# Optimization experiments

Hardware: AMD Instinct MI355X
Metric: run time of the kernel (lower is better)

Reference implementation:

```python
import jax, jax.numpy as jnp
import numpy as np

THETA = 0.5
LEAF_SIZE = 32
N_ATOMS = 8192
N_GRAPHS = 2


def _build_tree(pos_np, indices):
    # Mirrors OpenBoundaryTreeLongRangeKernel._build_tree (octree split at bbox center).
    local = pos_np[indices]
    cmin = local.min(axis=0)
    cmax = local.max(axis=0)
    center = 0.5 * (cmin + cmax)
    half = float((cmax - cmin).max() * 0.5)
    node = {"indices": indices, "iset": set(indices), "center": center,
            "half": half, "children": [], "cid": -1}
    if len(indices) <= LEAF_SIZE:
        return node
    bins = {}
    for i in indices:
        p = pos_np[i]
        key = (int(p[0] >= center[0]), int(p[1] >= center[1]), int(p[2] >= center[2]))
        bins.setdefault(key, []).append(i)
    if len(bins) <= 1:
        return node  # degenerate split -> treated as leaf (is_leaf == no children)
    node["children"] = [_build_tree(pos_np, ci) for ci in bins.values()]
    return node


def _plan(pos_np, batch_np, n_graphs, soft):
    # Host-side Barnes-Hut traversal (the torch original does this with .item() syncs).
    # Emits flat (target, source) direct pairs and (target, cluster) monopole pairs.
    direct_t, direct_s, clus_t, clus_c = [], [], [], []
    clusters = []
    for g in range(n_graphs):
        idx = np.nonzero(batch_np == g)[0]
        if idx.size == 0:
            continue
        root = _build_tree(pos_np, [int(i) for i in idx])
        for t in idx:
            t = int(t)
            tpos = pos_np[t]
            stack = [root]
            while stack:
                node = stack.pop()
                if not node["children"]:  # leaf: direct near-field sum
                    for s in node["indices"]:
                        if s != t:
                            direct_t.append(t)
                            direct_s.append(s)
                    continue
                d = tpos - node["center"]
                dist = float(np.sqrt((d * d).sum() + soft * soft))
                diam = max(2.0 * node["half"], 1e-9)
                if (t not in node["iset"]) and (diam / dist < THETA):
                    if node["cid"] < 0:
                        node["cid"] = len(clusters)
                        clusters.append(node["indices"])
                    clus_t.append(t)
                    clus_c.append(node["cid"])
                else:
                    stack.extend(node["children"])
    if clusters:
        midx = np.concatenate([np.asarray(c, dtype=np.int32) for c in clusters])
        mseg = np.concatenate([np.full(len(c), i, np.int32) for i, c in enumerate(clusters)])
        mcnt = np.asarray([len(c) for c in clusters], dtype=np.float32)
    else:
        midx = np.zeros((0,), np.int32)
        mseg = np.zeros((0,), np.int32)
        mcnt = np.ones((1,), np.float32)
    return (np.asarray(direct_t, np.int32), np.asarray(direct_s, np.int32),
            np.asarray(clus_t, np.int32), np.asarray(clus_c, np.int32),
            midx, mseg, mcnt, max(len(clusters), 1))


def _energy(pos, source, screening, softening, plan, n_atoms):
    # Vectorized, differentiable evaluation of the planned interactions.
    dt, ds, ct, cc, midx, mseg, mcnt, n_clusters = plan
    soft2 = softening * softening
    phi = jnp.zeros((n_atoms,), dtype=pos.dtype)
    if dt.size:
        delta = pos[dt] - pos[ds]                       # [P,3]
        r = jnp.sqrt(jnp.sum(delta * delta, axis=-1) + soft2)
        phi = phi + jax.ops.segment_sum(source[ds] * jnp.exp(-screening * r) / r,
                                        dt, num_segments=n_atoms)
    if ct.size:
        q = jax.ops.segment_sum(source[midx], mseg, num_segments=n_clusters)
        center = (jax.ops.segment_sum(pos[midx], mseg, num_segments=n_clusters)
                  / jnp.asarray(mcnt)[:, None])          # differentiable cluster mean
        delta = pos[ct] - center[cc]                    # [C,3]
        r = jnp.sqrt(jnp.sum(delta * delta, axis=-1) + soft2)
        phi = phi + jax.ops.segment_sum(q[cc] * jnp.exp(-screening * r) / r,
                                        ct, num_segments=n_atoms)
    return 0.5 * (source * phi)[:, None]                # [N,1], energy_partition='potential'


def setup_inputs() -> dict:
    key = jax.random.key(0)
    k1, k2, k3 = jax.random.split(key, 3)
    pos = jax.random.normal(k1, (N_ATOMS, 3), dtype=jnp.float32) * 6.0
    batch = jnp.sort(jax.random.randint(k2, (N_ATOMS,), 0, N_GRAPHS)).astype(jnp.int32)
    cell = jnp.zeros((N_GRAPHS, 3, 3), dtype=jnp.float32)
    source = jax.random.normal(k3, (N_ATOMS,), dtype=jnp.float32)
    screening = jnp.float32(0.5)
    softening = jnp.float32(0.1)
    return {"pos": pos, "batch": batch, "cell": cell, "source": source,
            "screening": screening, "softening": softening}


def reference(pos, batch, cell, source, screening, softening):
    pos_np = np.asarray(pos, dtype=np.float32)
    batch_np = np.asarray(batch)
    plan = _plan(pos_np, batch_np, int(cell.shape[0]), float(np.asarray(softening)))
    return _energy(pos, source, screening, softening, plan, pos.shape[0])
```

## Files before the change

kernel.cpp:

```cpp
#include <hip/hip_runtime.h>

#define LEAF_SZ 32
#define MAXN 16384
#define MAXNODES 65536
#define ARENA_BASE 32768
#define MAXG 64
#define NQ 1024
#define BGRID 128
#define LCAP 256
#define LSTK 192
#define BSTK 96
#define WQCAP 256
#define NW0 16

struct __align__(64) TNode { int4 meta; float4 c4; float4 m4; float4 pad; };

__device__ int    g_perm[MAXN];
__device__ int    g_ptmp[MAXN];
__device__ float4 g_p4[MAXN];
__device__ float4 g_t4[MAXN];
__device__ int    g_nstart[MAXNODES];
__device__ int    g_nend[MAXNODES];
__device__ TNode  g_nodes[MAXNODES];
__device__ int    g_root[MAXG];
__device__ int    g_ncount;
__device__ int    g_lrange[4];

struct NodeSh {
    float  mn[4][3], mx[4][3];
    double sx[4], sy[4], sz[4], sq[4];
    int    c8[4][8];
    int    cur[8];
    float  cc[3];
    int    info;
    int    base, num;
    int    tot[8], offk[8];
};

__device__ __forceinline__ void process_node2(NodeSh& sh, int n, int st, int en)
{
    const int tid  = threadIdx.x;
    const int wid  = tid >> 6;
    const int lane = tid & 63;
    const int cnt = en - st;

    float mnx = 3.402823466e38f, mny = mnx, mnz = mnx;
    float mxx = -mnx, mxy = -mnx, mxz = -mnx;
    double sx = 0.0, sy = 0.0, sz = 0.0, sq = 0.0;
    for (int j = st + tid; j < en; j += 256) {
        float4 p = g_p4[j];
        mnx = fminf(mnx, p.x); mny = fminf(mny, p.y); mnz = fminf(mnz, p.z);
        mxx = fmaxf(mxx, p.x); mxy = fmaxf(mxy, p.y); mxz = fmaxf(mxz, p.z);
        sx += (double)p.x; sy += (double)p.y; sz += (double)p.z; sq += (double)p.w;
    }
    for (int o = 1; o < 64; o <<= 1) {
        mnx = fminf(mnx, __shfl_xor(mnx, o));
        mny = fminf(mny, __shfl_xor(mny, o));
        mnz = fminf(mnz, __shfl_xor(mnz, o));
        mxx = fmaxf(mxx, __shfl_xor(mxx, o));
        mxy = fmaxf(mxy, __shfl_xor(mxy, o));
        mxz = fmaxf(mxz, __shfl_xor(mxz, o));
        sx += __shfl_xor(sx, o);
        sy += __shfl_xor(sy, o);
        sz += __shfl_xor(sz, o);
        sq += __shfl_xor(sq, o);
    }
    if (lane == 0) {
        sh.mn[wid][0] = mnx; sh.mn[wid][1] = mny; sh.mn[wid][2] = mnz;
        sh.mx[wid][0] = mxx; sh.mx[wid][1] = mxy; sh.mx[wid][2] = mxz;
        sh.sx[wid] = sx; sh.sy[wid] = sy; sh.sz[wid] = sz; sh.sq[wid] = sq;
    }
    __syncthreads();
    if (tid == 0) {
        float a0 = sh.mn[0][0], a1 = sh.mn[0][1], a2 = sh.mn[0][2];
        float b0 = sh.mx[0][0], b1 = sh.mx[0][1], b2 = sh.mx[0][2];
        double tx = sh.sx[0], ty = sh.sy[0], tz = sh.sz[0], tq = sh.sq[0];
        for (int w = 1; w < 4; ++w) {
            a0 = fminf(a0, sh.mn[w][0]); a1 = fminf(a1, sh.mn[w][1]); a2 = fminf(a2, sh.mn[w][2]);
            b0 = fmaxf(b0, sh.mx[w][0]); b1 = fmaxf(b1, sh.mx[w][1]); b2 = fmaxf(b2, sh.mx[w][2]);
            tx += sh.sx[w]; ty += sh.sy[w]; tz += sh.sz[w]; tq += sh.sq[w];
        }
        float cx = 0.5f * (a0 + b0), cy = 0.5f * (a1 + b1), cz = 0.5f * (a2 + b2);
        g_nodes[n].c4 = make_float4(cx, cy, cz, 0.5f * fmaxf(fmaxf(b0 - a0, b1 - a1), b2 - a2));
        const float fc = (float)cnt;
        g_nodes[n].m4 = make_float4((float)tx / fc, (float)ty / fc, (float)tz / fc, (float)tq);
        sh.cc[0] = cx; sh.cc[1] = cy; sh.cc[2] = cz;
        if (cnt <= LEAF_SZ) { g_nodes[n].meta = make_int4(st, en, 0, 0); sh.info = -1; }
        else sh.info = 0;
    }
    __syncthreads();
    if (sh.info < 0) return;
    const float cx = sh.cc[0], cy = sh.cc[1], cz = sh.cc[2];

    int c8[8] = {0,0,0,0,0,0,0,0};
    for (int j = st + tid; j < en; j += 256) {
        float4 p = g_p4[j];
        int oct = (p.x >= cx ? 1 : 0) | (p.y >= cy ? 2 : 0) | (p.z >= cz ? 4 : 0);
        c8[oct]++;
    }
    #pragma unroll
    for (int k = 0; k < 8; ++k)
        for (int o = 1; o < 64; o <<= 1)
            c8[k] += __shfl_xor(c8[k], o);
    if (lane == 0)
        #pragma unroll
        for (int k = 0; k < 8; ++k) sh.c8[wid][k] = c8[k];
    __syncthreads();
    if (tid == 0) {
        int tot[8], nonempty = 0;
        #pragma unroll
        for (int k = 0; k < 8; ++k) {
            tot[k] = sh.c8[0][k] + sh.c8[1][k] + sh.c8[2][k] + sh.c8[3][k];
            nonempty += (tot[k] > 0) ? 1 : 0;
        }
        if (nonempty <= 1) { g_nodes[n].meta = make_int4(st, en, 0, 0); sh.info = -1; }
        else {
            int base = atomicAdd(&g_ncount, nonempty);
            int acc = st, ci = base;
            #pragma unroll
            for (int k = 0; k < 8; ++k) {
                sh.cur[k] = acc;
                sh.offk[k] = acc - st;
                sh.tot[k] = tot[k];
                if (tot[k] > 0) { g_nstart[ci] = acc; g_nend[ci] = acc + tot[k]; ++ci; }
                acc += tot[k];
            }
            g_nodes[n].meta = make_int4(st, en, base, nonempty);
            sh.base = base; sh.num = nonempty; sh.info = 1;
        }
    }
    __syncthreads();
    if (sh.info < 0) return;

    for (int j = st + tid; j < en; j += 256) {
        float4 p = g_p4[j];
        int id = g_perm[j];
        int oct = (p.x >= cx ? 1 : 0) | (p.y >= cy ? 2 : 0) | (p.z >= cz ? 4 : 0);
        int pdst = atomicAdd(&sh.cur[oct], 1);
        g_ptmp[pdst] = id; g_t4[pdst] = p;
    }
    __syncthreads();
    for (int j = st + tid; j < en; j += 256) {
        g_perm[j] = g_ptmp[j];
        g_p4[j]   = g_t4[j];
    }
    __syncthreads();
}

__global__ __launch_bounds__(1024)
void level0_kernel(const float* __restrict__ pos, const float* __restrict__ src,
                   const int* __restrict__ batch, int N, int n_graphs)
{
    __shared__ int    s_first[MAXG], s_end[MAXG];
    __shared__ float  s_mn[NW0][3], s_mx[NW0][3];
    __shared__ double s_sx[NW0], s_sy[NW0], s_sz[NW0], s_sq[NW0];
    __shared__ int    s_c8[NW0][8];
    __shared__ int    s_cur[8];
    __shared__ float  s_cc[3];
    __shared__ int    s_info;
    const int tid = threadIdx.x, wid = tid >> 6, lane = tid & 63;
    const int ng = (n_graphs < MAXG) ? n_graphs : MAXG;

    for (int g = tid; g < MAXG; g += 1024) { s_first[g] = -1; s_end[g] = 0; }
    __syncthreads();
    for (int i = tid; i < N; i += 1024) {
        int b = batch[i];
        if (i == 0     || batch[i-1] != b) s_first[b] = i;
        if (i == N - 1 || batch[i+1] != b) s_end[b]   = i + 1;
    }
    __syncthreads();

    const int g = blockIdx.x;
    int nc = 0, myroot = -1;
    for (int q = 0; q < ng; ++q)
        if (s_first[q] >= 0) { if (q == g) myroot = nc; ++nc; }
    const int nb = nc + 8 * ng;

    if (g == 0 && tid == 0) {
        int r = 0;
        for (int q = 0; q < ng; ++q) {
            if (s_first[q] >= 0) g_root[q] = r++;
            else {
                g_root[q] = -1;
                for (int c = 0; c < 8; ++c) g_nstart[nc + q*8 + c] = -1;
            }
        }
        g_ncount = nb;
        g_lrange[0] = nc;
        g_lrange[1] = nb;
    }
    if (g >= ng || myroot < 0) return;

    const int st = s_first[g], en = s_end[g];
    const int cnt = en - st;
    const int n = myroot;
    const int cbase = nc + g * 8;

    float mnx = 3.402823466e38f, mny = mnx, mnz = mnx;
    float mxx = -mnx, mxy = -mnx, mxz = -mnx;
    double sx = 0.0, sy = 0.0, sz = 0.0, sq = 0.0;
    for (int j = st + tid; j < en; j += 1024) {
        float x = pos[3*j], y = pos[3*j+1], z = pos[3*j+2], s = src[j];
        mnx = fminf(mnx, x); mny = fminf(mny, y); mnz = fminf(mnz, z);
        mxx = fmaxf(mxx, x); mxy = fmaxf(mxy, y); mxz = fmaxf(mxz, z);
        sx += (double)x; sy += (double)y; sz += (double)z; sq += (double)s;
    }
    for (int o = 1; o < 64; o <<= 1) {
        mnx = fminf(mnx, __shfl_xor(mnx, o));
        mny = fminf(mny, __shfl_xor(mny, o));
        mnz = fminf(mnz, __shfl_xor(mnz, o));
        mxx = fmaxf(mxx, __shfl_xor(mxx, o));
        mxy = fmaxf(mxy, __shfl_xor(mxy, o));
        mxz = fmaxf(mxz, __shfl_xor(mxz, o));
        sx += __shfl_xor(sx, o);
        sy += __shfl_xor(sy, o);
        sz += __shfl_xor(sz, o);
        sq += __shfl_xor(sq, o);
    }
    if (lane == 0) {
        s_mn[wid][0] = mnx; s_mn[wid][1] = mny; s_mn[wid][2] = mnz;
        s_mx[wid][0] = mxx; s_mx[wid][1] = mxy; s_mx[wid][2] = mxz;
        s_sx[wid] = sx; s_sy[wid] = sy; s_sz[wid] = sz; s_sq[wid] = sq;
    }
    __syncthreads();
    if (tid == 0) {
        float a0 = s_mn[0][0], a1 = s_mn[0][1], a2 = s_mn[0][2];
        float b0 = s_mx[0][0], b1 = s_mx[0][1], b2 = s_mx[0][2];
        double tx = s_sx[0], ty = s_sy[0], tz = s_sz[0], tq = s_sq[0];
        for (int w = 1; w < NW0; ++w) {
            a0 = fminf(a0, s_mn[w][0]); a1 = fminf(a1, s_mn[w][1]); a2 = fminf(a2, s_mn[w][2]);
            b0 = fmaxf(b0, s_mx[w][0]); b1 = fmaxf(b1, s_mx[w][1]); b2 = fmaxf(b2, s_mx[w][2]);
            tx += s_sx[w]; ty += s_sy[w]; tz += s_sz[w]; tq += s_sq[w];
        }
        float cx = 0.5f * (a0 + b0), cy = 0.5f * (a1 + b1), cz = 0.5f * (a2 + b2);
        g_nodes[n].c4 = make_float4(cx, cy, cz, 0.5f * fmaxf(fmaxf(b0 - a0, b1 - a1), b2 - a2));
        const float fc = (float)cnt;
        g_nodes[n].m4 = make_float4((float)tx / fc, (float)ty / fc, (float)tz / fc, (float)tq);
        s_cc[0] = cx; s_cc[1] = cy; s_cc[2] = cz;
        s_info = (cnt <= LEAF_SZ) ? -1 : 0;
        if (s_info < 0) g_nodes[n].meta = make_int4(st, en, 0, 0);
    }
    __syncthreads();

    if (s_info == 0) {
        const float cx = s_cc[0], cy = s_cc[1], cz = s_cc[2];
        int c8[8] = {0,0,0,0,0,0,0,0};
        for (int j = st + tid; j < en; j += 1024) {
            int oct = (pos[3*j] >= cx ? 1 : 0) | (pos[3*j+1] >= cy ? 2 : 0) | (pos[3*j+2] >= cz ? 4 : 0);
            c8[oct]++;
        }
        #pragma unroll
        for (int k = 0; k < 8; ++k)
            for (int o = 1; o < 64; o <<= 1)
                c8[k] += __shfl_xor(c8[k], o);
        if (lane == 0)
            #pragma unroll
            for (int k = 0; k < 8; ++k) s_c8[wid][k] = c8[k];
        __syncthreads();
        if (tid == 0) {
            int tot[8], nonempty = 0;
            #pragma unroll
            for (int k = 0; k < 8; ++k) {
                int tk = 0;
                for (int w = 0; w < NW0; ++w) tk += s_c8[w][k];
                tot[k] = tk;
                nonempty += (tk > 0) ? 1 : 0;
            }
            if (nonempty <= 1) {
                g_nodes[n].meta = make_int4(st, en, 0, 0);
                for (int c = 0; c < 8; ++c) g_nstart[cbase + c] = -1;
                s_info = -1;
            } else {
                int acc = st, ci = cbase;
                #pragma unroll
                for (int k = 0; k < 8; ++k) {
                    s_cur[k] = acc;
                    if (tot[k] > 0) { g_nstart[ci] = acc; g_nend[ci] = acc + tot[k]; ++ci; }
                    acc += tot[k];
                }
                for (int c = ci; c < cbase + 8; ++c) g_nstart[c] = -1;
                g_nodes[n].meta = make_int4(st, en, cbase, nonempty);
                s_info = 1;
            }
        }
        __syncthreads();
    } else if (tid == 0) {
        for (int c = 0; c < 8; ++c) g_nstart[cbase + c] = -1;
    }

    if (s_info == 1) {
        const float cx = s_cc[0], cy = s_cc[1], cz = s_cc[2];
        for (int j = st + tid; j < en; j += 1024) {
            float x = pos[3*j], y = pos[3*j+1], z = pos[3*j+2], s = src[j];
            int oct = (x >= cx ? 1 : 0) | (y >= cy ? 2 : 0) | (z >= cz ? 4 : 0);
            int pdst = atomicAdd(&s_cur[oct], 1);
            g_p4[pdst] = make_float4(x, y, z, s);
            g_perm[pdst] = j;
        }
    } else {
        for (int j = st + tid; j < en; j += 1024) {
            g_p4[j] = make_float4(pos[3*j], pos[3*j+1], pos[3*j+2], src[j]);
            g_perm[j] = j;
        }
    }
}

__device__ __forceinline__ void lds_subtree(int rootn, int st, int en, int abase,
                                            float4* a4, int* aid,
                                            int* lid, int* la, int* lbb)
{
    const int lane = threadIdx.x & 63;
    const int cnt = en - st;
    const unsigned long long mlt = (1ull << lane) - 1ull;

    for (int j = lane; j < cnt; j += 64) {
        a4[j]  = g_p4[st + j];
        aid[j] = g_perm[st + j];
    }
    asm volatile("s_waitcnt vmcnt(0) lgkmcnt(0)" ::: "memory");
    __builtin_amdgcn_wave_barrier();

    int sp = 0;
    int cn = rootn, ca = 0, cb = cnt;
    while (true) {
        const int c = cb - ca;
        float4 pv[4]; int idv[4]; int oc[4];
        float mnx = 3.402823466e38f, mny = mnx, mnz = mnx;
        float mxx = -mnx, mxy = -mnx, mxz = -mnx;
        float sx = 0.f, sy = 0.f, sz = 0.f, sq = 0.f;
        #pragma unroll
        for (int i = 0; i < 4; ++i) {
            bool act = (i*64 + lane) < c;
            int j = act ? (ca + i*64 + lane) : ca;
            float4 p = a4[j];
            pv[i] = p; idv[i] = aid[j];
            if (act) {
                mnx = fminf(mnx, p.x); mny = fminf(mny, p.y); mnz = fminf(mnz, p.z);
                mxx = fmaxf(mxx, p.x); mxy = fmaxf(mxy, p.y); mxz = fmaxf(mxz, p.z);
                sx += p.x; sy += p.y; sz += p.z; sq += p.w;
            }
        }
        for (int o = 1; o < 64; o <<= 1) {
            mnx = fminf(mnx, __shfl_xor(mnx, o));
            mny = fminf(mny, __shfl_xor(mny, o));
            mnz = fminf(mnz, __shfl_xor(mnz, o));
            mxx = fmaxf(mxx, __shfl_xor(mxx, o));
            mxy = fmaxf(mxy, __shfl_xor(mxy, o));
            mxz = fmaxf(mxz, __shfl_xor(mxz, o));
            sx += __shfl_xor(sx, o);
            sy += __shfl_xor(sy, o);
            sz += __shfl_xor(sz, o);
            sq += __shfl_xor(sq, o);
        }
        const float cx = 0.5f * (mnx + mxx);
        const float cy = 0.5f * (mny + mxy);
        const float cz = 0.5f * (mnz + mxz);
        if (lane == 0) {
            g_nodes[cn].c4 = make_float4(cx, cy, cz, 0.5f * fmaxf(fmaxf(mxx - mnx, mxy - mny), mxz - mnz));
            const float fc = (float)c;
            g_nodes[cn].m4 = make_float4(sx / fc, sy / fc, sz / fc, sq);
        }

        int nonempty = 0;
        int c8[8] = {0,0,0,0,0,0,0,0};
        if (c > LEAF_SZ) {
            #pragma unroll
            for (int i = 0; i < 4; ++i) {
                bool act = (i*64 + lane) < c;
                int o = act ? ((pv[i].x >= cx ? 1 : 0) | (pv[i].y >= cy ? 2 : 0) | (pv[i].z >= cz ? 4 : 0)) : 8;
                oc[i] = o;
                #pragma unroll
                for (int k = 0; k < 8; ++k)
                    c8[k] += (int)__popcll(__ballot(o == k));
            }
            #pragma unroll
            for (int k = 0; k < 8; ++k) nonempty += (c8[k] > 0) ? 1 : 0;
        }

        if (c <= LEAF_SZ || nonempty <= 1) {
            if (lane == 0) g_nodes[cn].meta = make_int4(st + ca, st + cb, 0, 0);
        } else {
            int off[8], acc = 0;
            #pragma unroll
            for (int k = 0; k < 8; ++k) { off[k] = acc; acc += c8[k]; }
            if (lane == 0) g_nodes[cn].meta = make_int4(st + ca, st + cb, abase, nonempty);
            int cum[8] = {0,0,0,0,0,0,0,0};
            #pragma unroll
            for (int i = 0; i < 4; ++i) {
                int o = oc[i];
                int pdst = 0;
                #pragma unroll
                for (int k = 0; k < 8; ++k) {
                    unsigned long long b = __ballot(o == k);
                    if (o == k) pdst = ca + off[k] + cum[k] + (int)__popcll(b & mlt);
                    cum[k] += (int)__popcll(b);
                }
                if (o < 8) { a4[pdst] = pv[i]; aid[pdst] = idv[i]; }
            }
            asm volatile("s_waitcnt lgkmcnt(0)" ::: "memory");
            __builtin_amdgcn_wave_barrier();
            if (lane == 0) {
                int ci = 0;
                #pragma unroll
                for (int k = 0; k < 8; ++k) {
                    if (c8[k] > 0) {
                        lid[sp + ci] = abase + ci;
                        la [sp + ci] = ca + off[k];
                        lbb[sp + ci] = ca + off[k] + c8[k];
                        ++ci;
                    }
                }
            }
            abase += nonempty; sp += nonempty;
            if (sp > LSTK) sp = LSTK;
        }
        if (sp <= 0) break;
        --sp;
        __builtin_amdgcn_wave_barrier();
        asm volatile("s_waitcnt lgkmcnt(0)" ::: "memory");
        cn = lid[sp]; ca = la[sp]; cb = lbb[sp];
        __builtin_amdgcn_wave_barrier();
    }

    for (int j = lane; j < cnt; j += 64) {
        g_p4[st + j]  = a4[j];
        g_perm[st + j] = aid[j];
    }
    asm volatile("s_waitcnt vmcnt(0)" ::: "memory");
}

__global__ __launch_bounds__(256) void block_subtree_kernel()
{
    __shared__ NodeSh sh;
    __shared__ int bs_id[BSTK], bs_st[BSTK], bs_en[BSTK];
    __shared__ int wq_id[WQCAP], wq_st[WQCAP], wq_en[WQCAP];
    __shared__ int s_bsp, s_wq;
    __shared__ float4 s_a4[4][LCAP];
    __shared__ int    s_aid[4][LCAP];
    __shared__ int    s_lid[4][LSTK], s_la[4][LSTK], s_lb[4][LSTK];

    const int tid = threadIdx.x;
    const int wid = tid >> 6;
    const int lb = g_lrange[0], le = g_lrange[1];

    for (int task = lb + blockIdx.x; task < le; task += BGRID) {
        __syncthreads();
        int tst = g_nstart[task];
        if (tst < 0) continue;
        if (tid == 0) {
            int en = g_nend[task];
            if (en - tst <= LCAP) { wq_id[0] = task; wq_st[0] = tst; wq_en[0] = en; s_wq = 1; s_bsp = 0; }
            else                  { bs_id[0] = task; bs_st[0] = tst; bs_en[0] = en; s_bsp = 1; s_wq = 0; }
        }
        __syncthreads();

        while (true) {
            __syncthreads();
            const int bsp = s_bsp;
            if (bsp == 0) break;
            const int n  = bs_id[bsp-1];
            const int st = bs_st[bsp-1];
            const int en = bs_en[bsp-1];
            __syncthreads();
            if (tid == 0) s_bsp = bsp - 1;
            process_node2(sh, n, st, en);
            if (tid == 0 && sh.info == 1) {
                int ci = 0;
                #pragma unroll
                for (int k = 0; k < 8; ++k) {
                    if (sh.tot[k] > 0) {
                        int cst = st + sh.offk[k], cen = cst + sh.tot[k];
                        int cid = sh.base + ci; ++ci;
                        if (cen - cst <= LCAP && s_wq < WQCAP) {
                            wq_id[s_wq] = cid; wq_st[s_wq] = cst; wq_en[s_wq] = cen; ++s_wq;
                        } else if (s_bsp < BSTK) {
                            bs_id[s_bsp] = cid; bs_st[s_bsp] = cst; bs_en[s_bsp] = cen; ++s_bsp;
                        }
                    }
                }
            }
        }
        __syncthreads();

        const int nwq = s_wq;
        float4* a4 = s_a4[wid];  int* aid = s_aid[wid];
        int* lid = s_lid[wid];   int* la = s_la[wid];  int* lbb = s_lb[wid];
        for (int i = wid; i < nwq; i += 4) {
            int cid = wq_id[i], cst = wq_st[i], cen = wq_en[i];
            lds_subtree(cid, cst, cen, ARENA_BASE + 2 * cst, a4, aid, lid, la, lbb);
        }
    }
}

__global__ __launch_bounds__(256)
void traverse_kernel(const int* __restrict__ batch,
                     const float* __restrict__ p_scr, const float* __restrict__ p_soft,
                     float* __restrict__ out, int N)
{
    __shared__ int s_q[4][NQ];
    __shared__ int s_sb[4][64], s_ss[4][64], s_mk[4][64];
    __shared__ int s_qt[4];
    const int wid  = threadIdx.x >> 6;
    const int lane = threadIdx.x & 63;
    const int slot = blockIdx.x * 4 + wid;
    if (slot >= N) return;
    const int t = g_perm[slot];

    const float scr   = p_scr[0];
    const float soft  = p_soft[0];
    const float soft2 = soft * soft;
    const float cexp  = -scr * 1.4426950408889634f;
    const float4 tp = g_p4[slot];
    const float tx = tp.x, ty = tp.y, tz = tp.z;
    const int inv_t = slot;

    volatile int* q = s_q[wid];
    int* sb = s_sb[wid];
    int* ss = s_ss[wid];
    int* mk = s_mk[wid];
    if (lane == 0) { q[0] = g_root[batch[t]]; s_qt[wid] = 1; }
    __builtin_amdgcn_wave_barrier();

    float phi = 0.f;
    int qh = 0;
    while (true) {
        __builtin_amdgcn_wave_barrier();
        int qt = ((volatile int*)s_qt)[wid];
        if (qh >= qt) break;
        int take = qt - qh; if (take > 64) take = 64;
        int node = (lane < take) ? q[(qh + lane) & (NQ - 1)] : -1;
        qh += take;

        int leaf_st = 0, leaf_cnt = 0;
        if (node >= 0) {
            const int4 meta = g_nodes[node].meta;
            if (meta.w == 0) {
                leaf_st = meta.x; leaf_cnt = meta.y - meta.x;
            } else {
                float4 c4 = g_nodes[node].c4;
                float dx = tx - c4.x, dy = ty - c4.y, dz = tz - c4.z;
                float dist = sqrtf(dx*dx + dy*dy + dz*dz + soft2);
                float diam = fmaxf(2.0f * c4.w, 1e-9f);
                bool inside = (inv_t >= meta.x) && (inv_t < meta.y);
                if (!inside && diam < 0.5f * dist) {
                    float4 m4 = g_nodes[node].m4;
                    float ax = tx - m4.x, ay = ty - m4.y, az = tz - m4.z;
                    float s = ax*ax + ay*ay + az*az + soft2;
                    float rinv = rsqrtf(s);
                    phi += m4.w * exp2f(cexp * (s * rinv)) * rinv;
                } else {
                    int p = atomicAdd(&s_qt[wid], meta.w);
                    for (int c = 0; c < meta.w; ++c) q[(p + c) & (NQ - 1)] = meta.z + c;
                }
            }
        }

        bool hasself = (inv_t >= leaf_st) && (inv_t < leaf_st + leaf_cnt);
        int cnt_adj = leaf_cnt - (hasself ? 1 : 0);
        int x = cnt_adj;
        #pragma unroll
        for (int o = 1; o < 64; o <<= 1) { int y = __shfl_up(x, o); if (lane >= o) x += y; }
        int total = __shfl(x, 63);
        int off = x - cnt_adj;

        if (total > 0) {
            sb[lane] = leaf_st - off;
            ss[lane] = hasself ? (off + (inv_t - leaf_st)) : 0x7fffffff;
            asm volatile("s_waitcnt lgkmcnt(0)" ::: "memory");
            __builtin_amdgcn_wave_barrier();
            int carry = -1;
            for (int cb = 0; cb < total; cb += 64) {
                mk[lane] = -1;
                asm volatile("s_waitcnt lgkmcnt(0)" ::: "memory");
                __builtin_amdgcn_wave_barrier();
                if (cnt_adj > 0 && off >= cb && off < cb + 64) mk[off - cb] = lane;
                asm volatile("s_waitcnt lgkmcnt(0)" ::: "memory");
                __builtin_amdgcn_wave_barrier();
                int own = mk[lane];
                if (lane == 0) own = own > carry ? own : carry;
                #pragma unroll
                for (int o = 1; o < 64; o <<= 1) {
                    int y = __shfl_up(own, o);
                    if (lane >= o) own = own > y ? own : y;
                }
                carry = __shfl(own, 63);
                int p = cb + lane;
                if (p < total) {
                    int j = sb[own] + p + ((p >= ss[own]) ? 1 : 0);
                    float4 pp = g_p4[j];
                    float dx = tx - pp.x, dy = ty - pp.y, dz = tz - pp.z;
                    float s = dx*dx + dy*dy + dz*dz + soft2;
                    float rinv = rsqrtf(s);
                    phi += pp.w * exp2f(cexp * (s * rinv)) * rinv;
                }
                __builtin_amdgcn_wave_barrier();
            }
        }
    }

    #pragma unroll
    for (int o = 1; o < 64; o <<= 1) phi += __shfl_xor(phi, o);
    if (lane == 0) out[t] = 0.5f * (tp.w * phi);
}

extern "C" void kernel_launch(void* const* d_in, const int* in_sizes, int n_in,
                              void* d_out, int out_size, void* d_ws, size_t ws_size,
                              hipStream_t stream) {
    const float* pos    = (const float*)d_in[0];
    const int*   batch  = (const int*)  d_in[1];
    const float* source = (const float*)d_in[3];
    const float* p_scr  = (const float*)d_in[4];
    const float* p_soft = (const float*)d_in[5];

    const int N        = in_sizes[0] / 3;
    const int n_graphs = in_sizes[2] / 9;

    int g0 = n_graphs > 0 ? n_graphs : 1;
    if (g0 > MAXG) g0 = MAXG;
    level0_kernel<<<g0, 1024, 0, stream>>>(pos, source, batch, N, n_graphs);
    block_subtree_kernel<<<BGRID, 256, 0, stream>>>();

    const int blocks = (N + 3) / 4;
    traverse_kernel<<<blocks, 256, 0, stream>>>(batch, p_scr, p_soft, (float*)d_out, N);
}
```

Measured before the change: 158.5 us.

## Split the first octree child level inside the level-0 block kernel

```diff
diff --git a/kernel.cpp b/kernel.cpp
--- a/kernel.cpp
+++ b/kernel.cpp
@@ -143,6 +143,119 @@
     for (int j = st + tid; j < en; j += 256) {
         g_perm[j] = g_ptmp[j];
         g_p4[j]   = g_t4[j];
+    }
+    __syncthreads();
+}
+
+__device__ __forceinline__ void process1024(
+    int n, int st, int en, int cb2,
+    float (*s_mn)[3], float (*s_mx)[3],
+    double* s_sx, double* s_sy, double* s_sz, double* s_sq,
+    int (*s_c8)[8], int* s_cur, float* s_cc, int* s_info)
+{
+    const int tid = threadIdx.x, wid = tid >> 6, lane = tid & 63;
+    const int cnt = en - st;
+
+    float mnx = 3.402823466e38f, mny = mnx, mnz = mnx;
+    float mxx = -mnx, mxy = -mnx, mxz = -mnx;
+    double sx = 0.0, sy = 0.0, sz = 0.0, sq = 0.0;
+    for (int j = st + tid; j < en; j += 1024) {
+        float4 p = g_p4[j];
+        mnx = fminf(mnx, p.x); mny = fminf(mny, p.y); mnz = fminf(mnz, p.z);
+        mxx = fmaxf(mxx, p.x); mxy = fmaxf(mxy, p.y); mxz = fmaxf(mxz, p.z);
+        sx += (double)p.x; sy += (double)p.y; sz += (double)p.z; sq += (double)p.w;
+    }
+    for (int o = 1; o < 64; o <<= 1) {
+        mnx = fminf(mnx, __shfl_xor(mnx, o));
+        mny = fminf(mny, __shfl_xor(mny, o));
+        mnz = fminf(mnz, __shfl_xor(mnz, o));
+        mxx = fmaxf(mxx, __shfl_xor(mxx, o));
+        mxy = fmaxf(mxy, __shfl_xor(mxy, o));
+        mxz = fmaxf(mxz, __shfl_xor(mxz, o));
+        sx += __shfl_xor(sx, o);
+        sy += __shfl_xor(sy, o);
+        sz += __shfl_xor(sz, o);
+        sq += __shfl_xor(sq, o);
+    }
+    if (lane == 0) {
+        s_mn[wid][0] = mnx; s_mn[wid][1] = mny; s_mn[wid][2] = mnz;
+        s_mx[wid][0] = mxx; s_mx[wid][1] = mxy; s_mx[wid][2] = mxz;
+        s_sx[wid] = sx; s_sy[wid] = sy; s_sz[wid] = sz; s_sq[wid] = sq;
+    }
+    __syncthreads();
+    if (tid == 0) {
+        float a0 = s_mn[0][0], a1 = s_mn[0][1], a2 = s_mn[0][2];
+        float b0 = s_mx[0][0], b1 = s_mx[0][1], b2 = s_mx[0][2];
+        double tx = s_sx[0], ty = s_sy[0], tz = s_sz[0], tq = s_sq[0];
+        for (int w = 1; w < NW0; ++w) {
+            a0 = fminf(a0, s_mn[w][0]); a1 = fminf(a1, s_mn[w][1]); a2 = fminf(a2, s_mn[w][2]);
+            b0 = fmaxf(b0, s_mx[w][0]); b1 = fmaxf(b1, s_mx[w][1]); b2 = fmaxf(b2, s_mx[w][2]);
+            tx += s_sx[w]; ty += s_sy[w]; tz += s_sz[w]; tq += s_sq[w];
+        }
+        float cx = 0.5f * (a0 + b0), cy = 0.5f * (a1 + b1), cz = 0.5f * (a2 + b2);
+        g_nodes[n].c4 = make_float4(cx, cy, cz, 0.5f * fmaxf(fmaxf(b0 - a0, b1 - a1), b2 - a2));
+        const float fc = (float)cnt;
+        g_nodes[n].m4 = make_float4((float)tx / fc, (float)ty / fc, (float)tz / fc, (float)tq);
+        s_cc[0] = cx; s_cc[1] = cy; s_cc[2] = cz;
+        *s_info = (cnt <= LEAF_SZ) ? -1 : 0;
+        if (*s_info < 0) g_nodes[n].meta = make_int4(st, en, 0, 0);
+    }
+    __syncthreads();
+    if (*s_info < 0) return;
+    const float cx = s_cc[0], cy = s_cc[1], cz = s_cc[2];
+
+    int c8[8] = {0,0,0,0,0,0,0,0};
+    for (int j = st + tid; j < en; j += 1024) {
+        float4 p = g_p4[j];
+        int oct = (p.x >= cx ? 1 : 0) | (p.y >= cy ? 2 : 0) | (p.z >= cz ? 4 : 0);
+        c8[oct]++;
+    }
+    #pragma unroll
+    for (int k = 0; k < 8; ++k)
+        for (int o = 1; o < 64; o <<= 1)
+            c8[k] += __shfl_xor(c8[k], o);
+    if (lane == 0)
+        #pragma unroll
+        for (int k = 0; k < 8; ++k) s_c8[wid][k] = c8[k];
+    __syncthreads();
+    if (tid == 0) {
+        int tot[8], nonempty = 0;
+        #pragma unroll
+        for (int k = 0; k < 8; ++k) {
+            int tk = 0;
+            for (int w = 0; w < NW0; ++w) tk += s_c8[w][k];
+            tot[k] = tk;
+            nonempty += (tk > 0) ? 1 : 0;
+        }
+        if (nonempty <= 1) {
+            g_nodes[n].meta = make_int4(st, en, 0, 0);
+            *s_info = -1;
+        } else {
+            int acc = st, ci = cb2;
+            #pragma unroll
+            for (int k = 0; k < 8; ++k) {
+                s_cur[k] = acc;
+                if (tot[k] > 0) { g_nstart[ci] = acc; g_nend[ci] = acc + tot[k]; ++ci; }
+                acc += tot[k];
+            }
+            g_nodes[n].meta = make_int4(st, en, cb2, nonempty);
+            *s_info = 1;
+        }
+    }
+    __syncthreads();
+    if (*s_info < 0) return;
+
+    for (int j = st + tid; j < en; j += 1024) {
+        float4 p = g_p4[j];
+        int id = g_perm[j];
+        int oct = (p.x >= cx ? 1 : 0) | (p.y >= cy ? 2 : 0) | (p.z >= cz ? 4 : 0);
+        int pdst = atomicAdd(&s_cur[oct], 1);
+        g_t4[pdst] = p; g_ptmp[pdst] = id;
+    }
+    __syncthreads();
+    for (int j = st + tid; j < en; j += 1024) {
+        g_p4[j]   = g_t4[j];
+        g_perm[j] = g_ptmp[j];
     }
     __syncthreads();
 }
@@ -174,7 +287,8 @@
     int nc = 0, myroot = -1;
     for (int q = 0; q < ng; ++q)
         if (s_first[q] >= 0) { if (q == g) myroot = nc; ++nc; }
-    const int nb = nc + 8 * ng;
+    const int nb    = nc + 8 * ng;
+    const int l2end = nb + 64 * ng;
 
     if (g == 0 && tid == 0) {
         int r = 0;
@@ -182,14 +296,17 @@
             if (s_first[q] >= 0) g_root[q] = r++;
             else {
                 g_root[q] = -1;
-                for (int c = 0; c < 8; ++c) g_nstart[nc + q*8 + c] = -1;
-            }
-        }
-        g_ncount = nb;
-        g_lrange[0] = nc;
+                for (int c = 0; c < 8;  ++c) g_nstart[nc + q*8  + c] = -1;
+                for (int c = 0; c < 64; ++c) g_nstart[nb + q*64 + c] = -1;
+            }
+        }
+        g_ncount    = l2end;
         g_lrange[1] = nb;
+        g_lrange[2] = l2end;
     }
     if (g >= ng || myroot < 0) return;
+
+    for (int c = tid; c < 64; c += 1024) g_nstart[nb + g*64 + c] = -1;
 
     const int st = s_first[g], en = s_end[g];
     const int cnt = en - st;
@@ -302,6 +419,15 @@
             g_p4[j] = make_float4(pos[3*j], pos[3*j+1], pos[3*j+2], src[j]);
             g_perm[j] = j;
         }
+    }
+    __syncthreads();
+
+    for (int c = 0; c < 8; ++c) {
+        int cn  = cbase + c;
+        int cst = g_nstart[cn];
+        if (cst < 0) continue;
+        process1024(cn, cst, g_nend[cn], nb + g*64 + c*8,
+                    s_mn, s_mx, s_sx, s_sy, s_sz, s_sq, s_c8, s_cur, s_cc, &s_info);
     }
 }
 
@@ -441,7 +567,7 @@
 
     const int tid = threadIdx.x;
     const int wid = tid >> 6;
-    const int lb = g_lrange[0], le = g_lrange[1];
+    const int lb = g_lrange[1], le = g_lrange[2];
 
     for (int task = lb + blockIdx.x; task < le; task += BGRID) {
         __syncthreads();
```

Result: slower. 217.4 us (+37.2%).
